# Kernel tuning notes

Hardware: AMD Instinct MI355X
Metric: run time of the kernel (lower is better)

Reference implementation:

```python
import jax, jax.numpy as jnp
import numpy as np

B, S, N_LM, MAX_LEN = 32, 384, 543, 384

_FACE = [33, 133, 362, 263, 61, 291, 199, 419, 17, 84, 314, 405, 320, 307, 375, 321, 308, 324, 318]
_SEL = np.array(_FACE + list(range(468, 489)) + list(range(522, 543)) + [11, 12, 13, 14, 15, 16], dtype=np.int32)  # 67 landmarks
# pairwise distance index pairs: i in range(3), j in i+1..min(i+3, L)
_PAIRS = [(0, 1), (0, 2), (1, 2), (1, 3), (2, 3), (2, 4)]


def setup_inputs() -> dict:
    key = jax.random.key(0)
    x = jax.random.normal(key, (B, S, N_LM, 3), dtype=jnp.float32)
    return {"x": x}


def _safe_norm(v):
    # torch.norm(v + 1e-8, dim=-1, keepdim=True)
    w = v + 1e-8
    return jnp.sqrt(jnp.sum(w * w, axis=-1, keepdims=True))


def reference(x):
    # select 67 landmarks, keep xy only (z never enters the feature stack)
    c = x[:, :, _SEL, :2]                                  # (B,S,67,2)
    # per-frame masked mean-centering (inputs are finite -> plain mean)
    c = c - jnp.mean(c, axis=2, keepdims=True)
    # per-frame std over flattened (L*2) values, unbiased (torch.std)
    bsz, seq, L, _ = c.shape
    std = jnp.std(c.reshape(bsz, seq, -1), axis=-1, ddof=1)  # (B,S)
    scale = jnp.where(std > 1e-6, 1.0 / std, 1.0)[:, :, None, None]
    c = c * scale                                          # (B,S,67,2)

    zrow = jnp.zeros((bsz, 1, L, 2), c.dtype)
    vel = jnp.concatenate([zrow, c[:, 1:] - c[:, :-1]], axis=1)
    acc = jnp.concatenate([jnp.zeros((bsz, 2, L, 2), c.dtype), vel[:, 2:] - vel[:, 1:-1]], axis=1)

    vm = _safe_norm(vel)                                   # (B,S,67,1)
    am = _safe_norm(acc)
    # cum[t] = sum_{k<t} vm[k]
    cum = jnp.concatenate([jnp.zeros((bsz, 1, L, 1), c.dtype), jnp.cumsum(vm[:, :-1], axis=1)], axis=1)

    ang = jnp.arctan2(vel[..., 1:2] + 1e-8, vel[..., 0:1] + 1e-8)
    dchg = jnp.concatenate([jnp.zeros((bsz, 2, L, 1), c.dtype), ang[:, 2:] - ang[:, 1:-1]], axis=1)

    dists = jnp.concatenate([_safe_norm(c[:, :, i] - c[:, :, j]) for i, j in _PAIRS], axis=-1)  # (B,S,6)

    flat = lambda a: a.reshape(bsz, seq, -1)
    feats = jnp.concatenate([flat(c), flat(vel), flat(acc), flat(vm), flat(am), flat(cum), flat(ang), flat(dchg), dists], axis=-1)
    feats = jnp.where(jnp.isfinite(feats), feats, 0.0)
    return feats[:, :MAX_LEN]
```

## Files before the change

kernel.cpp:

```cpp
#include <hip/hip_runtime.h>
#include <math.h>

#define NB 32
#define NS 384
#define NLM 543
#define NL 67
#define NF 743

__constant__ int d_SEL[NL] = {
    33, 133, 362, 263, 61, 291, 199, 419, 17, 84, 314, 405, 320, 307, 375, 321, 308, 324, 318,
    468, 469, 470, 471, 472, 473, 474, 475, 476, 477, 478, 479, 480, 481, 482, 483, 484, 485, 486, 487, 488,
    522, 523, 524, 525, 526, 527, 528, 529, 530, 531, 532, 533, 534, 535, 536, 537, 538, 539, 540, 541, 542,
    11, 12, 13, 14, 15, 16
};

__device__ __forceinline__ float fin(float v) { return isfinite(v) ? v : 0.0f; }


__device__ __forceinline__ void gather_norm(const float* __restrict__ xr,
                                            int o0, int o1, bool has1,
                                            float& c0x, float& c0y,
                                            float& c1x, float& c1y) {
    float a0x = xr[o0], a0y = xr[o0 + 1];
    float a1x = 0.f, a1y = 0.f;
    if (has1) { a1x = xr[o1]; a1y = xr[o1 + 1]; }

    float sx = a0x + a1x, sy = a0y + a1y;
    #pragma unroll
    for (int off = 32; off; off >>= 1) { sx += __shfl_xor(sx, off); sy += __shfl_xor(sy, off); }
    const float mx = sx * (1.0f / 67.0f), my = sy * (1.0f / 67.0f);

    c0x = a0x - mx; c0y = a0y - my;
    c1x = a1x - mx; c1y = a1y - my;

    float ss = c0x * c0x + c0y * c0y + (has1 ? (c1x * c1x + c1y * c1y) : 0.f);
    #pragma unroll
    for (int off = 32; off; off >>= 1) ss += __shfl_xor(ss, off);
    const float stdv = sqrtf(ss * (1.0f / 133.0f));
    const float scale = (stdv > 1e-6f) ? (1.0f / stdv) : 1.0f;

    c0x *= scale; c0y *= scale; c1x *= scale; c1y *= scale;
}

__global__ __launch_bounds__(512) void k_main(const float* __restrict__ x,
                                              float* __restrict__ out,
                                              float* __restrict__ vmstage) {
    __shared__ float2 csh[10][NL];

    const int wave = threadIdx.x >> 6;
    const int lane = threadIdx.x & 63;
    const int b = blockIdx.x / 48;
    const int s_base = (blockIdx.x - b * 48) * 8;
    const int s = s_base + wave;
    const int bs = b * NS + s;

    const int lm0 = lane;
    const bool has1 = (lane < 3);
    const int lm1 = lane + 64;
    const int o0 = d_SEL[lm0] * 3;
    const int o1 = has1 ? d_SEL[lm1] * 3 : 0;

    const float* __restrict__ xb = x + (size_t)(b * NS) * (NLM * 3);

    float c0x, c0y, c1x, c1y;
    gather_norm(xb + (size_t)s * (NLM * 3), o0, o1, has1, c0x, c0y, c1x, c1y);
    csh[wave + 2][lm0] = make_float2(c0x, c0y);
    if (has1) csh[wave + 2][lm1] = make_float2(c1x, c1y);

    if (wave == 0) {
        if (s_base >= 1) {
            float bx, by, b1x, b1y;
            gather_norm(xb + (size_t)(s_base - 1) * (NLM * 3), o0, o1, has1, bx, by, b1x, b1y);
            csh[1][lm0] = make_float2(bx, by);
            if (has1) csh[1][lm1] = make_float2(b1x, b1y);
        } else {
            csh[1][lm0] = make_float2(0.f, 0.f);
            if (has1) csh[1][lm1] = make_float2(0.f, 0.f);
        }
    }
    if (wave == 1) {
        if (s_base >= 2) {
            float bx, by, b1x, b1y;
            gather_norm(xb + (size_t)(s_base - 2) * (NLM * 3), o0, o1, has1, bx, by, b1x, b1y);
            csh[0][lm0] = make_float2(bx, by);
            if (has1) csh[0][lm1] = make_float2(b1x, b1y);
        } else {
            csh[0][lm0] = make_float2(0.f, 0.f);
            if (has1) csh[0][lm1] = make_float2(0.f, 0.f);
        }
    }
    __syncthreads();

    float* __restrict__ row = out + (size_t)bs * NF;

    #pragma unroll
    for (int half = 0; half < 2; ++half) {
        if (half == 1 && !has1) break;
        const int lm = half ? lm1 : lm0;
        const float cx = half ? c1x : c0x, cy = half ? c1y : c0y;
        const float2 p = csh[wave + 1][lm];
        const float2 q = csh[wave][lm];

        const float vx = (s >= 1) ? (cx - p.x) : 0.f;
        const float vy = (s >= 1) ? (cy - p.y) : 0.f;
        const float v1x = p.x - q.x, v1y = p.y - q.y;
        const float ax = (s >= 2) ? (vx - v1x) : 0.f;
        const float ay = (s >= 2) ? (vy - v1y) : 0.f;

        const float wx = vx + 1e-8f, wy = vy + 1e-8f;
        const float vm = sqrtf(wx * wx + wy * wy);
        const float ux = ax + 1e-8f, uy = ay + 1e-8f;
        const float am = sqrtf(ux * ux + uy * uy);

        const float ang = atan2f(vy + 1e-8f, vx + 1e-8f);
        float dchg = 0.f;
        if (s >= 2) dchg = ang - atan2f(v1y + 1e-8f, v1x + 1e-8f);

        row[2 * lm]       = fin(cx);
        row[2 * lm + 1]   = fin(cy);
        row[134 + 2 * lm] = vx;
        row[135 + 2 * lm] = vy;
        row[268 + 2 * lm] = ax;
        row[269 + 2 * lm] = ay;
        row[402 + lm]     = vm;
        row[469 + lm]     = am;
        row[603 + lm]     = fin(ang);
        row[670 + lm]     = fin(dchg);
        vmstage[((size_t)b * NL + lm) * NS + s] = vm;
    }

    const int PI_[6] = {0, 0, 1, 1, 2, 2};
    const int PJ_[6] = {1, 2, 2, 3, 3, 4};
    const int p = (lane < 6) ? lane : 0;
    float xi = __shfl(c0x, PI_[p]); float yi = __shfl(c0y, PI_[p]);
    float xj = __shfl(c0x, PJ_[p]); float yj = __shfl(c0y, PJ_[p]);
    if (lane < 6) {
        float dx = xi - xj + 1e-8f, dy = yi - yj + 1e-8f;
        row[737 + lane] = fin(sqrtf(dx * dx + dy * dy));
    }
}

__global__ __launch_bounds__(256) void k_scan(const float* __restrict__ vmstage,
                                              float* __restrict__ out) {
    const int gw = (int)((blockIdx.x * 256u + threadIdx.x) >> 6);
    const int lane = threadIdx.x & 63;
    const int b = gw / NL;
    const int lm = gw - b * NL;
    const float* __restrict__ src = vmstage + (size_t)gw * NS;

    float carry = 0.f;
    #pragma unroll
    for (int k = 0; k < 6; ++k) {
        const int t = k * 64 + lane;
        const float v = src[t];
        float incl = v;
        #pragma unroll
        for (int off = 1; off < 64; off <<= 1) {
            float y = __shfl_up(incl, off);
            if (lane >= off) incl += y;
        }
        out[((size_t)(b * NS + t)) * NF + 536 + lm] = fin(carry + (incl - v));
        carry += __shfl(incl, 63);
    }
}

extern "C" void kernel_launch(void* const* d_in, const int* in_sizes, int n_in,
                              void* d_out, int out_size, void* d_ws, size_t ws_size,
                              hipStream_t stream) {
    const float* x = (const float*)d_in[0];
    float* out = (float*)d_out;
    float* vmstage = (float*)d_ws;

    k_main<<<NB * (NS / 8), 512, 0, stream>>>(x, out, vmstage);
    k_scan<<<(NB * NL) / 4, 256, 0, stream>>>(vmstage, out);
}
```

Measured before the change: 131.6 us.

## Share angles via LDS, coalesce vm staging and scan output writes

The main kernel now stores per-frame angles in shared memory and takes the direction change from the neighbouring frame's angle, so each frame computes one atan2 instead of two. The velocity magnitudes for the cumulative-sum scan are staged in shared memory and written as contiguous 8-frame runs instead of strided per-frame stores. The scan kernel groups 9 landmarks per block, runs the scans into a shared buffer, then writes contiguous 9-float segments of each output row rather than single scattered floats. This costs an extra block barrier and more shared memory per block.

New measurement: 128.5 us. -2.4%, faster.

```diff
diff --git a/kernel.cpp b/kernel.cpp
--- a/kernel.cpp
+++ b/kernel.cpp
@@ -46,6 +46,8 @@
                                               float* __restrict__ out,
                                               float* __restrict__ vmstage) {
     __shared__ float2 csh[10][NL];
+    __shared__ float ang_sh[9][NL];
+    __shared__ float vm_sh[8][NL];
 
     const int wave = threadIdx.x >> 6;
     const int lane = threadIdx.x & 63;
@@ -93,6 +95,8 @@
 
     float* __restrict__ row = out + (size_t)bs * NF;
 
+    float ang0_own = 0.f, ang1_own = 0.f;
+
     #pragma unroll
     for (int half = 0; half < 2; ++half) {
         if (half == 1 && !has1) break;
@@ -113,8 +117,9 @@
         const float am = sqrtf(ux * ux + uy * uy);
 
         const float ang = atan2f(vy + 1e-8f, vx + 1e-8f);
-        float dchg = 0.f;
-        if (s >= 2) dchg = ang - atan2f(v1y + 1e-8f, v1x + 1e-8f);
+        if (half) ang1_own = ang; else ang0_own = ang;
+        ang_sh[wave + 1][lm] = ang;
+        vm_sh[wave][lm] = vm;
 
         row[2 * lm]       = fin(cx);
         row[2 * lm + 1]   = fin(cy);
@@ -125,8 +130,17 @@
         row[402 + lm]     = vm;
         row[469 + lm]     = am;
         row[603 + lm]     = fin(ang);
-        row[670 + lm]     = fin(dchg);
-        vmstage[((size_t)b * NL + lm) * NS + s] = vm;
+    }
+
+    if (wave == 0) {
+        float bvx = csh[1][lm0].x - csh[0][lm0].x;
+        float bvy = csh[1][lm0].y - csh[0][lm0].y;
+        ang_sh[0][lm0] = atan2f(bvy + 1e-8f, bvx + 1e-8f);
+        if (has1) {
+            bvx = csh[1][lm1].x - csh[0][lm1].x;
+            bvy = csh[1][lm1].y - csh[0][lm1].y;
+            ang_sh[0][lm1] = atan2f(bvy + 1e-8f, bvx + 1e-8f);
+        }
     }
 
     const int PI_[6] = {0, 0, 1, 1, 2, 2};
@@ -138,29 +152,67 @@
         float dx = xi - xj + 1e-8f, dy = yi - yj + 1e-8f;
         row[737 + lane] = fin(sqrtf(dx * dx + dy * dy));
     }
+
+    __syncthreads();
+
+    if (s >= 2) {
+        row[670 + lm0] = fin(ang0_own - ang_sh[wave][lm0]);
+        if (has1) row[670 + lm1] = fin(ang1_own - ang_sh[wave][lm1]);
+    } else {
+        row[670 + lm0] = 0.f;
+        if (has1) row[670 + lm1] = 0.f;
+    }
+
+    for (int t = threadIdx.x; t < NL * 8; t += 512) {
+        const int lm = t >> 3, s8 = t & 7;
+        vmstage[((size_t)b * NL + lm) * NS + s_base + s8] = vm_sh[s8][lm];
+    }
 }
 
 __global__ __launch_bounds__(256) void k_scan(const float* __restrict__ vmstage,
                                               float* __restrict__ out) {
-    const int gw = (int)((blockIdx.x * 256u + threadIdx.x) >> 6);
+    __shared__ float cum_sh[NS][9];
+
+    const int b = blockIdx.x >> 3;
+    const int g = blockIdx.x & 7;
+    const int lm0 = g * 9;
+    const int cnt = (g == 7) ? 4 : 9;
+    const int wave = threadIdx.x >> 6;
     const int lane = threadIdx.x & 63;
-    const int b = gw / NL;
-    const int lm = gw - b * NL;
-    const float* __restrict__ src = vmstage + (size_t)gw * NS;
-
-    float carry = 0.f;
-    #pragma unroll
-    for (int k = 0; k < 6; ++k) {
-        const int t = k * 64 + lane;
-        const float v = src[t];
-        float incl = v;
+
+    for (int j = wave; j < cnt; j += 4) {
+        const float* __restrict__ src = vmstage + ((size_t)b * NL + lm0 + j) * NS;
+        float v[6];
         #pragma unroll
-        for (int off = 1; off < 64; off <<= 1) {
-            float y = __shfl_up(incl, off);
-            if (lane >= off) incl += y;
-        }
-        out[((size_t)(b * NS + t)) * NF + 536 + lm] = fin(carry + (incl - v));
-        carry += __shfl(incl, 63);
+        for (int k = 0; k < 6; ++k) v[k] = src[k * 64 + lane];
+        float carry = 0.f;
+        #pragma unroll
+        for (int k = 0; k < 6; ++k) {
+            float incl = v[k];
+            #pragma unroll
+            for (int off = 1; off < 64; off <<= 1) {
+                float y = __shfl_up(incl, off);
+                if (lane >= off) incl += y;
+            }
+            cum_sh[k * 64 + lane][j] = carry + (incl - v[k]);
+            carry += __shfl(incl, 63);
+        }
+    }
+    __syncthreads();
+
+    const int total = NS * cnt;
+    if (cnt == 9) {
+        for (int idx = threadIdx.x; idx < total; idx += 256) {
+            const int ss = idx / 9;
+            const int j = idx - ss * 9;
+            out[((size_t)(b * NS + ss)) * NF + 536 + lm0 + j] = fin(cum_sh[ss][j]);
+        }
+    } else {
+        for (int idx = threadIdx.x; idx < total; idx += 256) {
+            const int ss = idx >> 2;
+            const int j = idx & 3;
+            out[((size_t)(b * NS + ss)) * NF + 536 + lm0 + j] = fin(cum_sh[ss][j]);
+        }
     }
 }
 
@@ -172,5 +224,5 @@
     float* vmstage = (float*)d_ws;
 
     k_main<<<NB * (NS / 8), 512, 0, stream>>>(x, out, vmstage);
-    k_scan<<<(NB * NL) / 4, 256, 0, stream>>>(vmstage, out);
-}
+    k_scan<<<NB * 8, 256, 0, stream>>>(vmstage, out);
+}
```
